# Kernel optimization log

Measured on AMD Instinct MI355X. Metric: run time of the kernel, lower is better.

Reference implementation:

```python
import jax, jax.numpy as jnp
import numpy as np

RES = 64; UP = 128; LATENT = 16; RGB_LAT = 15
XYZ_MIN = -1.0; XYZ_MAX = 1.0
STEPSIZE = 0.5; NEAR = 0.2; FAR = 6.0; BG = 1.0
VOXEL = (XYZ_MAX - XYZ_MIN) / RES
ALPHA_INIT = 1e-4
ACT_SHIFT = float(np.log(1.0 / (1.0 - ALPHA_INIT) - 1.0))
N_SAMPLES = int(np.linalg.norm(np.array([2 * RES + 1] * 3)) / STEPSIZE) + 1
BN_SCALE = (1.0 + 1e-5) ** -0.5  # eval-mode BatchNorm with running_mean=0, running_var=1
EPS = 1e-12
FREQS = [float(2.0 ** i) for i in range(6)]

def _sobel_kernel():
    hd = np.array([-1., -2., 0., 2., 1.]); h = np.array([1., 4., 6., 4., 1.])
    kx = np.einsum('i,j,k->ijk', hd, h, h)
    ky = np.einsum('i,j,k->ijk', h, hd, h)
    kz = np.einsum('i,j,k->ijk', h, h, hd)
    K = np.stack([kx, ky, kz])[:, None]
    return jnp.asarray(K / np.abs(K).max(), dtype=jnp.float32)

SOBEL_K = _sobel_kernel()

def _normalize(x, axis=-1):
    return x / jnp.maximum(jnp.linalg.norm(x, axis=axis, keepdims=True), EPS)

def _conv1x1(x, w, b):
    return jnp.einsum('oc,cdhw->odhw', w, x) + b[:, None, None, None]

def _bn(x, g, b):
    return x * (BN_SCALE * g)[:, None, None, None] + b[:, None, None, None]

def _prelu(x, a):
    return jnp.where(x >= 0, x, a[:, None, None, None] * x)

def _grid_reg(grid, c1_w, c1_b, bn1_g, bn1_b, pr1_a, c2_w, c2_b, bn2_g, bn2_b, pr2_a, c3_w, c3_b):
    x1 = _prelu(_bn(_conv1x1(grid, c1_w, c1_b), bn1_g, bn1_b), pr1_a)
    x2 = _prelu(_bn(_conv1x1(jnp.concatenate([x1, grid], 0), c2_w, c2_b), bn2_g, bn2_b), pr2_a)
    x3 = _conv1x1(jnp.concatenate([x1, x2, grid], 0), c3_w, c3_b)  # [(1+15)*8, R, R, R]
    # PixelShuffle3d(scale=2): [16*8,R,R,R] -> [16,2R,2R,2R]
    up = x3.reshape(LATENT, 2, 2, 2, RES, RES, RES).transpose(0, 4, 1, 5, 2, 6, 3).reshape(LATENT, UP, UP, UP)
    sob = jax.lax.conv_general_dilated(up[:1][None], SOBEL_K, (1, 1, 1), [(2, 2)] * 3,
                                       dimension_numbers=('NCDHW', 'OIDHW', 'NCDHW'))[0]
    normals = -_normalize(sob, axis=0)
    return up.transpose(1, 2, 3, 0), normals.transpose(1, 2, 3, 0)  # [UP,UP,UP,16], [UP,UP,UP,3]

def _trilinear(feat, p):
    # feat: [UP,UP,UP,C] indexed as world (x,y,z); p: [...,3] world coords. align_corners=True.
    u = jnp.clip((p - XYZ_MIN) / (XYZ_MAX - XYZ_MIN) * (UP - 1), 0.0, UP - 1.0)
    i0 = jnp.clip(jnp.floor(u).astype(jnp.int32), 0, UP - 2)
    f = u - i0.astype(u.dtype)
    ix, iy, iz = i0[..., 0], i0[..., 1], i0[..., 2]
    fx, fy, fz = f[..., 0:1], f[..., 1:2], f[..., 2:3]
    def g(dx, dy, dz):
        return feat[ix + dx, iy + dy, iz + dz]
    c00 = g(0, 0, 0) * (1 - fz) + g(0, 0, 1) * fz
    c01 = g(0, 1, 0) * (1 - fz) + g(0, 1, 1) * fz
    c10 = g(1, 0, 0) * (1 - fz) + g(1, 0, 1) * fz
    c11 = g(1, 1, 0) * (1 - fz) + g(1, 1, 1) * fz
    c0 = c00 * (1 - fy) + c01 * fy
    c1 = c10 * (1 - fy) + c11 * fy
    return c0 * (1 - fx) + c1 * fx

def _sample_ray(rays_o, rays_d):
    vec = jnp.where(rays_d == 0, 1e-6, rays_d)
    rate_a = (XYZ_MAX - rays_o) / vec
    rate_b = (XYZ_MIN - rays_o) / vec
    t_min = jnp.clip(jnp.minimum(rate_a, rate_b).max(-1), NEAR, FAR)
    t_max = jnp.clip(jnp.maximum(rate_a, rate_b).min(-1), NEAR, FAR)
    mask_ray = t_max <= t_min
    rng = jnp.arange(N_SAMPLES, dtype=rays_o.dtype)  # eval mode: no jitter
    step = STEPSIZE * VOXEL * rng
    interpx = t_min[:, None] + step[None] / jnp.linalg.norm(rays_d, axis=-1, keepdims=True)
    pts = rays_o[:, None, :] + rays_d[:, None, :] * interpx[..., None]
    outbox = mask_ray[:, None] | ((pts < XYZ_MIN) | (pts > XYZ_MAX)).any(-1)
    return pts, outbox

def _forward(rays_o, rays_d, viewdirs, grid, c1_w, c1_b, bn1_g, bn1_b, pr1_a, c2_w, c2_b, bn2_g, bn2_b, pr2_a, c3_w, c3_b, mlp_w0, mlp_b0, mlp_w1, mlp_b1, mlp_w2, mlp_b2, mlp_w3, mlp_b3):
    feat_grid, normals_grid = _grid_reg(grid, c1_w, c1_b, bn1_g, bn1_b, pr1_a, c2_w, c2_b, bn2_g, bn2_b, pr2_a, c3_w, c3_b)
    pts, outbox = _sample_ray(rays_o, rays_d)
    inside = ~outbox
    N, S = pts.shape[:2]
    pf = pts.reshape(-1, 3)

    def alpha_fn(p):
        d = _trilinear(feat_grid, p)[..., 0]
        return 1.0 - jnp.exp(-jax.nn.softplus(d + ACT_SHIFT) * STEPSIZE)

    alpha_flat, vjp_fn = jax.vjp(alpha_fn, pf)
    grads = vjp_fn(jnp.ones_like(alpha_flat))[0]  # d alpha / d point (analytic normals)
    nd = -_normalize(grads).reshape(N, S, 3)
    nd = jnp.where(inside[..., None], nd, 0.0)
    alpha = jnp.where(inside, alpha_flat.reshape(N, S), 0.0)

    feat = _trilinear(feat_grid, pf)
    rgb_latent = feat[:, 1:].reshape(N, S, RGB_LAT)

    ns = -_normalize(_trilinear(normals_grid, pf)).reshape(N, S, 3)  # sobel normals
    ns = jnp.where(inside[..., None], ns, 0.0)

    v = jnp.broadcast_to(viewdirs[:, None, :], nd.shape)
    dot = jnp.sum(-v * nd, -1, keepdims=True)
    refdirs = 2.0 * dot * nd + v
    emb = jnp.concatenate([refdirs] + [f(refdirs * fr) for fr in FREQS for f in (jnp.sin, jnp.cos)], -1)
    hfeat = jnp.concatenate([rgb_latent, emb], -1)  # [N,S,54]
    h = jax.nn.relu(hfeat @ mlp_w0 + mlp_b0)
    h = jax.nn.relu(h @ mlp_w1 + mlp_b1)
    h = jax.nn.relu(h @ mlp_w2 + mlp_b2)
    rgb = jax.nn.sigmoid(h @ mlp_w3 + mlp_b3)
    rgb = jnp.where(inside[..., None], rgb, 0.0)

    t = jnp.cumprod(jnp.clip(1.0 - alpha, 1e-10, None), -1)
    alphainv = jnp.concatenate([jnp.ones_like(t[..., :1]), t], -1)
    weights = alpha * alphainv[..., :-1]
    rgb_m = (weights[..., None] * rgb).sum(-2) + alphainv[..., -1:] * BG
    depth = jnp.linalg.norm(rays_o[:, None, :] - pts, axis=-1)
    depth_m = (weights * depth).sum(-1) + alphainv[..., -1] * FAR
    disp = 1.0 / depth_m
    acc = weights.sum(-1)
    nm = (weights[..., None] * nd).sum(-2)
    sm = (weights[..., None] * ns).sum(-2)
    return jnp.concatenate([rgb_m, depth_m[..., None], disp[..., None], acc[..., None], nm, sm], -1)  # [N,12]

def setup_inputs() -> dict:
    key = jax.random.key(0)
    ks = jax.random.split(key, 16)
    N = 1024
    cam = jnp.array([0.0, 0.0, -2.5], dtype=jnp.float32)
    rays_o = cam + 0.05 * jax.random.normal(ks[0], (N, 3), dtype=jnp.float32)
    tgt = jax.random.uniform(ks[1], (N, 3), minval=-0.5, maxval=0.5, dtype=jnp.float32)
    d = tgt - rays_o
    viewdirs = d / jnp.linalg.norm(d, axis=-1, keepdims=True)
    def w(k, shape, s=0.1):
        return s * jax.random.normal(k, shape, dtype=jnp.float32)
    return dict(
        rays_o=rays_o, rays_d=d, viewdirs=viewdirs,
        grid=w(ks[2], (16, 64, 64, 64)),
        c1_w=w(ks[3], (64, 16)), c1_b=w(ks[4], (64,), 0.01),
        bn1_g=jnp.ones(64, jnp.float32), bn1_b=jnp.zeros(64, jnp.float32), pr1_a=0.25 * jnp.ones(64, jnp.float32),
        c2_w=w(ks[5], (64, 80)), c2_b=w(ks[6], (64,), 0.01),
        bn2_g=jnp.ones(64, jnp.float32), bn2_b=jnp.zeros(64, jnp.float32), pr2_a=0.25 * jnp.ones(64, jnp.float32),
        c3_w=w(ks[7], (128, 144)), c3_b=w(ks[8], (128,), 0.01),
        mlp_w0=w(ks[9], (54, 64)), mlp_b0=jnp.zeros(64, jnp.float32),
        mlp_w1=w(ks[10], (64, 64)), mlp_b1=jnp.zeros(64, jnp.float32),
        mlp_w2=w(ks[11], (64, 64)), mlp_b2=jnp.zeros(64, jnp.float32),
        mlp_w3=w(ks[12], (64, 3)), mlp_b3=jnp.zeros(3, jnp.float32))

def reference(rays_o, rays_d, viewdirs, grid, c1_w, c1_b, bn1_g, bn1_b, pr1_a, c2_w, c2_b, bn2_g, bn2_b, pr2_a, c3_w, c3_b, mlp_w0, mlp_b0, mlp_w1, mlp_b1, mlp_w2, mlp_b2, mlp_w3, mlp_b3):
    return _forward(rays_o, rays_d, viewdirs, grid, c1_w, c1_b, bn1_g, bn1_b, pr1_a, c2_w, c2_b, bn2_g, bn2_b, pr2_a, c3_w, c3_b, mlp_w0, mlp_b0, mlp_w1, mlp_b1, mlp_w2, mlp_b2, mlp_w3, mlp_b3)
```

## Files before the change

kernel.cpp:

```cpp
#include <hip/hip_runtime.h>
#include <math.h>

#define S_SAMPLES 447
#define ACT_SHIFT -9.210240366971207f
#define BN_SCALE_C 0.9999950000374997f
#define STEP_VOX 0.015625f

__device__ __forceinline__ unsigned f2bf_u(float f) {
    unsigned u = __float_as_uint(f);
    return (u + 0x7fffu + ((u >> 16) & 1u)) >> 16;
}
__device__ __forceinline__ float bf2f(unsigned short u) {
    return __uint_as_float(((unsigned)u) << 16);
}
__device__ __forceinline__ float bf_lo(unsigned u) { return __uint_as_float(u << 16); }
__device__ __forceinline__ float bf_hi(unsigned u) { return __uint_as_float(u & 0xffff0000u); }

typedef __attribute__((ext_vector_type(8))) short bf16x8;
typedef __attribute__((ext_vector_type(4))) float f32x4;

__global__ __launch_bounds__(256) void prep_kernel(
    const float* __restrict__ w1, const float* __restrict__ w2,
    const float* __restrict__ w3, const float* __restrict__ b3,
    const float* __restrict__ mw0, const float* __restrict__ mw1,
    const float* __restrict__ mw2,
    unsigned short* __restrict__ w1b, unsigned short* __restrict__ w2b,
    unsigned short* __restrict__ w3b, float* __restrict__ b3p,
    unsigned short* __restrict__ m0t, unsigned short* __restrict__ m1t,
    unsigned short* __restrict__ m2t)
{
    const int gid = blockIdx.x * 256 + threadIdx.x;
    const int gs = gridDim.x * 256;
    for (int idx = gid; idx < 2048; idx += gs) {
        const int o = idx >> 5, k = idx & 31;
        w1b[idx] = (k < 16) ? (unsigned short)f2bf_u(w1[o * 16 + k]) : 0;
    }
    for (int idx = gid; idx < 6144; idx += gs) {
        const int o = idx / 96, k = idx % 96;
        w2b[idx] = (k < 80) ? (unsigned short)f2bf_u(w2[o * 80 + k]) : 0;
    }
    for (int idx = gid; idx < 20480; idx += gs) {
        const int n = idx / 160, k = idx % 160;
        const int s = n >> 4, l = n & 15;
        const int o = l * 8 + s;
        float val = 0.f;
        if (k < 64)       val = w3[o * 144 + k];
        else if (k < 80)  val = w3[o * 144 + 128 + (k - 64)];
        else if (k >= 96) val = w3[o * 144 + 64 + (k - 96)];
        w3b[idx] = (unsigned short)f2bf_u(val);
    }
    for (int idx = gid; idx < 128; idx += gs) {
        const int o = idx;
        b3p[(o & 7) * 16 + (o >> 3)] = b3[o];
    }
    for (int idx = gid; idx < 4096; idx += gs) {
        const int o = idx >> 6, k = idx & 63;
        m0t[o * 64 + k] = (k < 54) ? (unsigned short)f2bf_u(mw0[k * 64 + o]) : 0;
    }
    for (int idx = gid; idx < 4096; idx += gs) {
        const int o = idx >> 6, k = idx & 63;
        m1t[o * 64 + k] = (unsigned short)f2bf_u(mw1[k * 64 + o]);
    }
    for (int idx = gid; idx < 4096; idx += gs) {
        const int o = idx >> 6, k = idx & 63;
        m2t[o * 64 + k] = (unsigned short)f2bf_u(mw2[k * 64 + o]);
    }
}

__global__ __launch_bounds__(64) void conv_fused_kernel(
    const float* __restrict__ grid,
    const unsigned short* __restrict__ w1b, const float* __restrict__ b1,
    const float* __restrict__ g1, const float* __restrict__ bb1, const float* __restrict__ a1,
    const unsigned short* __restrict__ w2b, const float* __restrict__ b2,
    const float* __restrict__ g2, const float* __restrict__ bb2, const float* __restrict__ a2,
    const unsigned short* __restrict__ w3b, const float* __restrict__ b3p,
    unsigned short* __restrict__ featb, float* __restrict__ dens)
{
    __shared__ __align__(16) unsigned short AT[32 * 168];
    __shared__ float densT[32 * 8];
    unsigned short* Ct = AT;
    const int t = threadIdx.x;
    const int v0 = blockIdx.x * 32;

    for (int idx = t; idx < 256; idx += 64) {
        const int v = idx >> 3, c = idx & 7;
        *(unsigned*)(AT + v * 168 + 80 + c * 2) = 0;
    }
#pragma unroll
    for (int i = 0; i < 8; ++i) {
        const int c = 2 * i + (t >> 5);
        const float gv = grid[(size_t)c * 262144 + v0 + (t & 31)];
        AT[(t & 31) * 168 + 64 + c] = (unsigned short)f2bf_u(gv);
    }
    __syncthreads();

    const int quad = t >> 4, l16 = t & 15;

    {
        f32x4 acc[2][4];
        float gs[4], bb[4], al[4];
#pragma unroll
        for (int nt = 0; nt < 4; ++nt) {
            const int ch = 16 * nt + l16;
            const float bch = b1[ch];
            gs[nt] = BN_SCALE_C * g1[ch]; bb[nt] = bb1[ch]; al[nt] = a1[ch];
#pragma unroll
            for (int mt = 0; mt < 2; ++mt) {
                acc[mt][nt][0] = bch; acc[mt][nt][1] = bch;
                acc[mt][nt][2] = bch; acc[mt][nt][3] = bch;
            }
        }
        const int k0 = 8 * quad;
        bf16x8 a[2], b[4];
#pragma unroll
        for (int mt = 0; mt < 2; ++mt)
            a[mt] = __builtin_bit_cast(bf16x8, *(const uint4*)(AT + (16 * mt + l16) * 168 + 64 + k0));
#pragma unroll
        for (int nt = 0; nt < 4; ++nt)
            b[nt] = __builtin_bit_cast(bf16x8, *(const uint4*)(w1b + (16 * nt + l16) * 32 + k0));
#pragma unroll
        for (int mt = 0; mt < 2; ++mt)
#pragma unroll
            for (int nt = 0; nt < 4; ++nt)
                acc[mt][nt] = __builtin_amdgcn_mfma_f32_16x16x32_bf16(a[mt], b[nt], acc[mt][nt], 0, 0, 0);
        __syncthreads();
#pragma unroll
        for (int mt = 0; mt < 2; ++mt)
#pragma unroll
            for (int nt = 0; nt < 4; ++nt)
#pragma unroll
                for (int reg = 0; reg < 4; ++reg) {
                    float x = acc[mt][nt][reg] * gs[nt] + bb[nt];
                    x = (x >= 0.f) ? x : al[nt] * x;
                    AT[(16 * mt + 4 * quad + reg) * 168 + 16 * nt + l16] = (unsigned short)f2bf_u(x);
                }
    }
    __syncthreads();

    {
        f32x4 acc[2][4];
        float gs[4], bb[4], al[4];
#pragma unroll
        for (int nt = 0; nt < 4; ++nt) {
            const int ch = 16 * nt + l16;
            const float bch = b2[ch];
            gs[nt] = BN_SCALE_C * g2[ch]; bb[nt] = bb2[ch]; al[nt] = a2[ch];
#pragma unroll
            for (int mt = 0; mt < 2; ++mt) {
                acc[mt][nt][0] = bch; acc[mt][nt][1] = bch;
                acc[mt][nt][2] = bch; acc[mt][nt][3] = bch;
            }
        }
#pragma unroll
        for (int kq = 0; kq < 3; ++kq) {
            const int k0 = 32 * kq + 8 * quad;
            bf16x8 a[2], b[4];
#pragma unroll
            for (int mt = 0; mt < 2; ++mt)
                a[mt] = __builtin_bit_cast(bf16x8, *(const uint4*)(AT + (16 * mt + l16) * 168 + k0));
#pragma unroll
            for (int nt = 0; nt < 4; ++nt)
                b[nt] = __builtin_bit_cast(bf16x8, *(const uint4*)(w2b + (16 * nt + l16) * 96 + k0));
#pragma unroll
            for (int mt = 0; mt < 2; ++mt)
#pragma unroll
                for (int nt = 0; nt < 4; ++nt)
                    acc[mt][nt] = __builtin_amdgcn_mfma_f32_16x16x32_bf16(a[mt], b[nt], acc[mt][nt], 0, 0, 0);
        }
        __syncthreads();
#pragma unroll
        for (int mt = 0; mt < 2; ++mt)
#pragma unroll
            for (int nt = 0; nt < 4; ++nt)
#pragma unroll
                for (int reg = 0; reg < 4; ++reg) {
                    float x = acc[mt][nt][reg] * gs[nt] + bb[nt];
                    x = (x >= 0.f) ? x : al[nt] * x;
                    AT[(16 * mt + 4 * quad + reg) * 168 + 96 + 16 * nt + l16] = (unsigned short)f2bf_u(x);
                }
    }
    __syncthreads();

    {
        f32x4 acc[2][8];
#pragma unroll
        for (int nt = 0; nt < 8; ++nt) {
            const float bv = b3p[16 * nt + l16];
#pragma unroll
            for (int mt = 0; mt < 2; ++mt) {
                acc[mt][nt][0] = bv; acc[mt][nt][1] = bv;
                acc[mt][nt][2] = bv; acc[mt][nt][3] = bv;
            }
        }
#pragma unroll
        for (int kq = 0; kq < 5; ++kq) {
            const int k0 = 32 * kq + 8 * quad;
            bf16x8 a[2], b[8];
#pragma unroll
            for (int mt = 0; mt < 2; ++mt)
                a[mt] = __builtin_bit_cast(bf16x8, *(const uint4*)(AT + (16 * mt + l16) * 168 + k0));
#pragma unroll
            for (int nt = 0; nt < 8; ++nt)
                b[nt] = __builtin_bit_cast(bf16x8, *(const uint4*)(w3b + (size_t)(16 * nt + l16) * 160 + k0));
#pragma unroll
            for (int mt = 0; mt < 2; ++mt)
#pragma unroll
                for (int nt = 0; nt < 8; ++nt)
                    acc[mt][nt] = __builtin_amdgcn_mfma_f32_16x16x32_bf16(a[mt], b[nt], acc[mt][nt], 0, 0, 0);
        }

        __syncthreads();

        if (l16 == 0) {
#pragma unroll
            for (int mt = 0; mt < 2; ++mt)
#pragma unroll
                for (int nt = 0; nt < 8; ++nt)
#pragma unroll
                    for (int reg = 0; reg < 4; ++reg)
                        densT[(16 * mt + 4 * quad + reg) * 8 + nt] = acc[mt][nt][reg];
        }
#pragma unroll
        for (int mt = 0; mt < 2; ++mt)
#pragma unroll
            for (int nt = 0; nt < 8; ++nt)
#pragma unroll
                for (int reg = 0; reg < 4; ++reg)
                    Ct[(16 * mt + 4 * quad + reg) * 136 + 16 * nt + l16] =
                        (unsigned short)f2bf_u(acc[mt][nt][reg]);
    }
    __syncthreads();

    const int v = t >> 1, half = t & 1;
    const int vg = v0 + v;
    const int Z = vg & 63, Y = (vg >> 6) & 63, X = vg >> 12;
#pragma unroll
    for (int si = 0; si < 4; ++si) {
        const int s = 4 * half + si;
        const int d2 = (s >> 2) & 1, h2 = (s >> 1) & 1, w2i = s & 1;
        const int ubase = ((2 * X + d2) * 128 + (2 * Y + h2)) * 128 + (2 * Z + w2i);
        const uint4 q0 = *(const uint4*)(Ct + v * 136 + 16 * s);
        const uint4 q1 = *(const uint4*)(Ct + v * 136 + 16 * s + 8);
        *(uint4*)(featb + (size_t)ubase * 16)     = q0;
        *(uint4*)(featb + (size_t)ubase * 16 + 8) = q1;
        dens[ubase] = densT[v * 8 + s];
    }
}

__global__ __launch_bounds__(256) void sobelZ_kernel(const float* __restrict__ dens,
                                                     float2* __restrict__ zbuf)
{
    const int v = blockIdx.x * 256 + threadIdx.x;
    const int z = v & 127;
    float d[5];
#pragma unroll
    for (int k = 0; k < 5; ++k) {
        const int zz = z + k - 2;
        d[k] = (zz >= 0 && zz < 128) ? dens[v + (k - 2)] : 0.f;
    }
    const float az = d[0] + 4.f * d[1] + 6.f * d[2] + 4.f * d[3] + d[4];
    const float bz = -d[0] - 2.f * d[1] + 2.f * d[3] + d[4];
    zbuf[v] = make_float2(az, bz);
}

__global__ __launch_bounds__(256) void sobelY_kernel(const float2* __restrict__ zbuf,
                                                     float4* __restrict__ cbuf)
{
    const int v = blockIdx.x * 256 + threadIdx.x;
    const int y = (v >> 7) & 127;
    float2 e[5];
#pragma unroll
    for (int j = 0; j < 5; ++j) {
        const int yy = y + j - 2;
        e[j] = (yy >= 0 && yy < 128) ? zbuf[v + (j - 2) * 128] : make_float2(0.f, 0.f);
    }
    const float c1 = e[0].x + 4.f * e[1].x + 6.f * e[2].x + 4.f * e[3].x + e[4].x;
    const float c2 = -e[0].x - 2.f * e[1].x + 2.f * e[3].x + e[4].x;
    const float c3 = e[0].y + 4.f * e[1].y + 6.f * e[2].y + 4.f * e[3].y + e[4].y;
    cbuf[v] = make_float4(c1, c2, c3, 0.f);
}

__global__ __launch_bounds__(256) void sobelX_kernel(const float4* __restrict__ cbuf,
                                                     float* __restrict__ normals)
{
    const int v = blockIdx.x * 256 + threadIdx.x;
    const int x = v >> 14;
    float4 q[5];
#pragma unroll
    for (int i = 0; i < 5; ++i) {
        const int xx = x + i - 2;
        q[i] = (xx >= 0 && xx < 128) ? cbuf[v + (i - 2) * 16384]
                                     : make_float4(0.f, 0.f, 0.f, 0.f);
    }
    float sx = -q[0].x - 2.f * q[1].x + 2.f * q[3].x + q[4].x;
    float sy = q[0].y + 4.f * q[1].y + 6.f * q[2].y + 4.f * q[3].y + q[4].y;
    float sz = q[0].z + 4.f * q[1].z + 6.f * q[2].z + 4.f * q[3].z + q[4].z;
    sx *= (1.f / 72.f); sy *= (1.f / 72.f); sz *= (1.f / 72.f);
    const float n = sqrtf(sx * sx + sy * sy + sz * sz);
    const float inv = 1.f / fmaxf(n, 1e-12f);
    normals[v * 3 + 0] = -sx * inv;
    normals[v * 3 + 1] = -sy * inv;
    normals[v * 3 + 2] = -sz * inv;
}

__device__ __forceinline__ void mfma_layer(unsigned short* A,
                                           const unsigned short* __restrict__ Wg,
                                           const float* __restrict__ bias,
                                           const int lane)
{
    const int quad = lane >> 4, l16 = lane & 15;
    f32x4 acc[4][4];
#pragma unroll
    for (int nt = 0; nt < 4; ++nt) {
        const float bv = bias[16 * nt + l16];
#pragma unroll
        for (int mt = 0; mt < 4; ++mt) {
            acc[mt][nt][0] = bv; acc[mt][nt][1] = bv;
            acc[mt][nt][2] = bv; acc[mt][nt][3] = bv;
        }
    }
    bf16x8 a[2][4], b[2][4];
#pragma unroll
    for (int kq = 0; kq < 2; ++kq) {
        const int k0 = 32 * kq + 8 * quad;
#pragma unroll
        for (int mt = 0; mt < 4; ++mt)
            a[kq][mt] = __builtin_bit_cast(bf16x8, *(const uint4*)(A + (16 * mt + l16) * 72 + k0));
#pragma unroll
        for (int nt = 0; nt < 4; ++nt)
            b[kq][nt] = __builtin_bit_cast(bf16x8, *(const uint4*)(Wg + (16 * nt + l16) * 64 + k0));
    }
#pragma unroll
    for (int kq = 0; kq < 2; ++kq)
#pragma unroll
        for (int mt = 0; mt < 4; ++mt)
#pragma unroll
            for (int nt = 0; nt < 4; ++nt)
                acc[mt][nt] = __builtin_amdgcn_mfma_f32_16x16x32_bf16(a[kq][mt], b[kq][nt], acc[mt][nt], 0, 0, 0);
    __syncthreads();
#pragma unroll
    for (int mt = 0; mt < 4; ++mt)
#pragma unroll
        for (int nt = 0; nt < 4; ++nt)
#pragma unroll
            for (int reg = 0; reg < 4; ++reg) {
                const float v = fmaxf(acc[mt][nt][reg], 0.f);
                A[(16 * mt + 4 * quad + reg) * 72 + 16 * nt + l16] =
                    (unsigned short)f2bf_u(v);
            }
    __syncthreads();
}

__global__ __launch_bounds__(64) void sample_kernel(
    const float* __restrict__ ro, const float* __restrict__ rd, const float* __restrict__ vd,
    const unsigned short* __restrict__ featb, const float* __restrict__ dens,
    const float* __restrict__ normals,
    const unsigned short* __restrict__ m0t, const float* __restrict__ mb0,
    const unsigned short* __restrict__ m1t, const float* __restrict__ mb1,
    const unsigned short* __restrict__ m2t, const float* __restrict__ mb2,
    const float* __restrict__ mw3, const float* __restrict__ mb3,
    float* __restrict__ sbuf, const int total)
{
    __shared__ __align__(16) unsigned short act[64 * 72];

    const int t = threadIdx.x;
    const int s = blockIdx.x * 64 + t;
    const bool live = (s < total);
    bool actv = false;
    float alpha = 0.f, ndx = 0.f, ndy = 0.f, ndz = 0.f;
    float nsx = 0.f, nsy = 0.f, nsz = 0.f, depth = 0.f;
    float hf[64];
#pragma unroll
    for (int q = 0; q < 64; ++q) hf[q] = 0.f;

    if (live) {
        const int r = s / S_SAMPLES;
        const int j = s - r * S_SAMPLES;

        const float ox = ro[r * 3 + 0], oy = ro[r * 3 + 1], oz = ro[r * 3 + 2];
        const float dx = rd[r * 3 + 0], dy = rd[r * 3 + 1], dz = rd[r * 3 + 2];
        const float vx = vd[r * 3 + 0], vy = vd[r * 3 + 1], vz = vd[r * 3 + 2];

        const float vecx = (dx == 0.f) ? 1e-6f : dx;
        const float vecy = (dy == 0.f) ? 1e-6f : dy;
        const float vecz = (dz == 0.f) ? 1e-6f : dz;
        const float rax = (1.f - ox) / vecx, rbx = (-1.f - ox) / vecx;
        const float ray2 = (1.f - oy) / vecy, rby = (-1.f - oy) / vecy;
        const float raz = (1.f - oz) / vecz, rbz = (-1.f - oz) / vecz;
        float tmin = fmaxf(fmaxf(fminf(rax, rbx), fminf(ray2, rby)), fminf(raz, rbz));
        float tmax = fminf(fminf(fmaxf(rax, rbx), fmaxf(ray2, rby)), fmaxf(raz, rbz));
        tmin = fminf(fmaxf(tmin, 0.2f), 6.0f);
        tmax = fminf(fmaxf(tmax, 0.2f), 6.0f);
        const bool mask_ray = (tmax <= tmin);

        const float ndr = sqrtf(dx * dx + dy * dy + dz * dz);
        const float interpx = tmin + (STEP_VOX * (float)j) / ndr;
        const float px = ox + dx * interpx;
        const float py = oy + dy * interpx;
        const float pz = oz + dz * interpx;
        const bool outbox = mask_ray || (px < -1.f) || (px > 1.f) || (py < -1.f) ||
                            (py > 1.f) || (pz < -1.f) || (pz > 1.f);
        actv = !outbox;
        if (actv) {
            const float ux = fminf(fmaxf((px + 1.f) * 63.5f, 0.f), 127.f);
            const float uy = fminf(fmaxf((py + 1.f) * 63.5f, 0.f), 127.f);
            const float uz = fminf(fmaxf((pz + 1.f) * 63.5f, 0.f), 127.f);
            const int ix = min(max((int)floorf(ux), 0), 126);
            const int iy = min(max((int)floorf(uy), 0), 126);
            const int iz = min(max((int)floorf(uz), 0), 126);
            const float fx = ux - (float)ix, fy = uy - (float)iy, fz = uz - (float)iz;

            float lat[15];
#pragma unroll
            for (int q = 0; q < 15; ++q) lat[q] = 0.f;
            float na0 = 0.f, na1 = 0.f, na2 = 0.f;
            float c0v[8];
#pragma unroll
            for (int cn = 0; cn < 8; ++cn) {
                const int adx = cn >> 2, ady = (cn >> 1) & 1, adz = cn & 1;
                const int vox = ((ix + adx) * 128 + (iy + ady)) * 128 + (iz + adz);
                const float w = (adx ? fx : 1.f - fx) * (ady ? fy : 1.f - fy) * (adz ? fz : 1.f - fz);
                c0v[cn] = dens[vox];
                const uint4* cp = (const uint4*)(featb + (size_t)vox * 16);
                const uint4 q0 = cp[0], q1 = cp[1];
                lat[0]  = fmaf(w, bf_hi(q0.x), lat[0]);
                lat[1]  = fmaf(w, bf_lo(q0.y), lat[1]);
                lat[2]  = fmaf(w, bf_hi(q0.y), lat[2]);
                lat[3]  = fmaf(w, bf_lo(q0.z), lat[3]);
                lat[4]  = fmaf(w, bf_hi(q0.z), lat[4]);
                lat[5]  = fmaf(w, bf_lo(q0.w), lat[5]);
                lat[6]  = fmaf(w, bf_hi(q0.w), lat[6]);
                lat[7]  = fmaf(w, bf_lo(q1.x), lat[7]);
                lat[8]  = fmaf(w, bf_hi(q1.x), lat[8]);
                lat[9]  = fmaf(w, bf_lo(q1.y), lat[9]);
                lat[10] = fmaf(w, bf_hi(q1.y), lat[10]);
                lat[11] = fmaf(w, bf_lo(q1.z), lat[11]);
                lat[12] = fmaf(w, bf_hi(q1.z), lat[12]);
                lat[13] = fmaf(w, bf_lo(q1.w), lat[13]);
                lat[14] = fmaf(w, bf_hi(q1.w), lat[14]);
                const float* np_ = normals + (size_t)vox * 3;
                na0 = fmaf(w, np_[0], na0);
                na1 = fmaf(w, np_[1], na1);
                na2 = fmaf(w, np_[2], na2);
            }

            const float c00 = c0v[0] * (1.f - fz) + c0v[1] * fz;
            const float c01 = c0v[2] * (1.f - fz) + c0v[3] * fz;
            const float c10 = c0v[4] * (1.f - fz) + c0v[5] * fz;
            const float c11 = c0v[6] * (1.f - fz) + c0v[7] * fz;
            const float e0 = c00 * (1.f - fy) + c01 * fy;
            const float e1 = c10 * (1.f - fy) + c11 * fy;
            const float d0 = e0 * (1.f - fx) + e1 * fx;
            const float dfx = e1 - e0;
            const float dfy = (c01 - c00) * (1.f - fx) + (c11 - c10) * fx;
            const float dfz = ((c0v[1] - c0v[0]) * (1.f - fy) + (c0v[3] - c0v[2]) * fy) * (1.f - fx)
                            + ((c0v[5] - c0v[4]) * (1.f - fy) + (c0v[7] - c0v[6]) * fy) * fx;

            const float zin = d0 + ACT_SHIFT;
            const float splus = fmaxf(zin, 0.f) + log1pf(__expf(-fabsf(zin)));
            const float e = __expf(-splus * 0.5f);
            alpha = 1.f - e;
            const float sig = 1.f / (1.f + __expf(-zin));
            const float dad = e * 0.5f * sig;
            const float gx = dad * dfx * 63.5f;
            const float gy = dad * dfy * 63.5f;
            const float gz = dad * dfz * 63.5f;
            const float gn = sqrtf(gx * gx + gy * gy + gz * gz);
            const float gi = 1.f / fmaxf(gn, 1e-12f);
            ndx = -gx * gi; ndy = -gy * gi; ndz = -gz * gi;

            const float nn = sqrtf(na0 * na0 + na1 * na1 + na2 * na2);
            const float ni = 1.f / fmaxf(nn, 1e-12f);
            nsx = -na0 * ni; nsy = -na1 * ni; nsz = -na2 * ni;

            const float dotv = -(vx * ndx + vy * ndy + vz * ndz);
            const float rx = 2.f * dotv * ndx + vx;
            const float ry = 2.f * dotv * ndy + vy;
            const float rz = 2.f * dotv * ndz + vz;

#pragma unroll
            for (int q = 0; q < 15; ++q) hf[q] = lat[q];
            hf[15] = rx; hf[16] = ry; hf[17] = rz;
#pragma unroll
            for (int fi = 0; fi < 6; ++fi) {
                const float fr = (float)(1 << fi);
                hf[18 + fi * 6 + 0] = __sinf(rx * fr);
                hf[18 + fi * 6 + 1] = __sinf(ry * fr);
                hf[18 + fi * 6 + 2] = __sinf(rz * fr);
                hf[18 + fi * 6 + 3] = __cosf(rx * fr);
                hf[18 + fi * 6 + 4] = __cosf(ry * fr);
                hf[18 + fi * 6 + 5] = __cosf(rz * fr);
            }
            depth = interpx * ndr;
        }
    }

#pragma unroll
    for (int q = 0; q < 8; ++q) {
        uint4 st;
        st.x = f2bf_u(hf[8 * q + 0]) | (f2bf_u(hf[8 * q + 1]) << 16);
        st.y = f2bf_u(hf[8 * q + 2]) | (f2bf_u(hf[8 * q + 3]) << 16);
        st.z = f2bf_u(hf[8 * q + 4]) | (f2bf_u(hf[8 * q + 5]) << 16);
        st.w = f2bf_u(hf[8 * q + 6]) | (f2bf_u(hf[8 * q + 7]) << 16);
        *(uint4*)(act + t * 72 + 8 * q) = st;
    }
    __syncthreads();

    mfma_layer(act, m0t, mb0, t);
    mfma_layer(act, m1t, mb1, t);
    mfma_layer(act, m2t, mb2, t);

    if (live) {
        float* so = sbuf + (size_t)s * 12;
        if (actv) {
            float r0 = mb3[0], r1 = mb3[1], r2 = mb3[2];
            const unsigned short* hr = act + t * 72;
#pragma unroll
            for (int c8 = 0; c8 < 8; ++c8) {
                const uint4 hu = *(const uint4*)(hr + 8 * c8);
                const float h[8] = {bf_lo(hu.x), bf_hi(hu.x), bf_lo(hu.y), bf_hi(hu.y),
                                    bf_lo(hu.z), bf_hi(hu.z), bf_lo(hu.w), bf_hi(hu.w)};
#pragma unroll
                for (int u = 0; u < 8; ++u) {
                    const int c = 8 * c8 + u;
                    r0 = fmaf(h[u], mw3[c * 3 + 0], r0);
                    r1 = fmaf(h[u], mw3[c * 3 + 1], r1);
                    r2 = fmaf(h[u], mw3[c * 3 + 2], r2);
                }
            }
            so[0] = alpha;
            so[1] = 1.f / (1.f + __expf(-r0));
            so[2] = 1.f / (1.f + __expf(-r1));
            so[3] = 1.f / (1.f + __expf(-r2));
            so[4] = ndx; so[5] = ndy; so[6] = ndz;
            so[7] = nsx; so[8] = nsy; so[9] = nsz;
            so[10] = depth;
            so[11] = 0.f;
        } else {
#pragma unroll
            for (int q = 0; q < 12; ++q) so[q] = 0.f;
        }
    }
}

__global__ __launch_bounds__(64) void reduce_kernel(const float* __restrict__ sbuf,
                                                    float* __restrict__ out)
{
    const int r = blockIdx.x;
    const int lane = threadIdx.x;
    const int per = (S_SAMPLES + 63) / 64;
    const int j0 = lane * per;
    const int j1 = min(S_SAMPLES, j0 + per);

    float p = 1.f;
    for (int j = j0; j < j1; ++j) {
        const float a = sbuf[((size_t)r * S_SAMPLES + j) * 12];
        p *= fmaxf(1.f - a, 1e-10f);
    }
    float scan = p;
#pragma unroll
    for (int off = 1; off < 64; off <<= 1) {
        const float nv = __shfl_up(scan, (unsigned)off, 64);
        if (lane >= off) scan *= nv;
    }
    const float total = __shfl(scan, 63, 64);
    float pref = __shfl_up(scan, 1u, 64);
    if (lane == 0) pref = 1.f;

    float s0 = 0, s1 = 0, s2 = 0, s3 = 0, s4 = 0, s5 = 0, s6 = 0, s7 = 0, s8 = 0, s9 = 0, s10 = 0;
    for (int j = j0; j < j1; ++j) {
        const float* sp_ = sbuf + ((size_t)r * S_SAMPLES + j) * 12;
        const float a = sp_[0];
        const float w = a * pref;
        pref *= fmaxf(1.f - a, 1e-10f);
        s0 = fmaf(w, sp_[1], s0);
        s1 = fmaf(w, sp_[2], s1);
        s2 = fmaf(w, sp_[3], s2);
        s3 = fmaf(w, sp_[10], s3);
        s4 += w;
        s5 = fmaf(w, sp_[4], s5);
        s6 = fmaf(w, sp_[5], s6);
        s7 = fmaf(w, sp_[6], s7);
        s8 = fmaf(w, sp_[7], s8);
        s9 = fmaf(w, sp_[8], s9);
        s10 = fmaf(w, sp_[9], s10);
    }
#pragma unroll
    for (int m = 32; m >= 1; m >>= 1) {
        s0 += __shfl_xor(s0, m, 64);
        s1 += __shfl_xor(s1, m, 64);
        s2 += __shfl_xor(s2, m, 64);
        s3 += __shfl_xor(s3, m, 64);
        s4 += __shfl_xor(s4, m, 64);
        s5 += __shfl_xor(s5, m, 64);
        s6 += __shfl_xor(s6, m, 64);
        s7 += __shfl_xor(s7, m, 64);
        s8 += __shfl_xor(s8, m, 64);
        s9 += __shfl_xor(s9, m, 64);
        s10 += __shfl_xor(s10, m, 64);
    }
    if (lane == 0) {
        const float dm = s3 + total * 6.0f;
        out[r * 12 + 0] = s0 + total;
        out[r * 12 + 1] = s1 + total;
        out[r * 12 + 2] = s2 + total;
        out[r * 12 + 3] = dm;
        out[r * 12 + 4] = 1.f / dm;
        out[r * 12 + 5] = s4;
        out[r * 12 + 6] = s5; out[r * 12 + 7] = s6; out[r * 12 + 8] = s7;
        out[r * 12 + 9] = s8; out[r * 12 + 10] = s9; out[r * 12 + 11] = s10;
    }
}

extern "C" void kernel_launch(void* const* d_in, const int* in_sizes, int n_in,
                              void* d_out, int out_size, void* d_ws, size_t ws_size,
                              hipStream_t stream)
{
    (void)n_in; (void)out_size; (void)ws_size;
    const float* rays_o   = (const float*)d_in[0];
    const float* rays_d   = (const float*)d_in[1];
    const float* viewdirs = (const float*)d_in[2];
    const float* grid     = (const float*)d_in[3];
    const float* c1_w  = (const float*)d_in[4];
    const float* c1_b  = (const float*)d_in[5];
    const float* bn1_g = (const float*)d_in[6];
    const float* bn1_b = (const float*)d_in[7];
    const float* pr1_a = (const float*)d_in[8];
    const float* c2_w  = (const float*)d_in[9];
    const float* c2_b  = (const float*)d_in[10];
    const float* bn2_g = (const float*)d_in[11];
    const float* bn2_b = (const float*)d_in[12];
    const float* pr2_a = (const float*)d_in[13];
    const float* c3_w  = (const float*)d_in[14];
    const float* c3_b  = (const float*)d_in[15];
    const float* mw0 = (const float*)d_in[16];
    const float* mb0 = (const float*)d_in[17];
    const float* mw1 = (const float*)d_in[18];
    const float* mb1 = (const float*)d_in[19];
    const float* mw2 = (const float*)d_in[20];
    const float* mb2 = (const float*)d_in[21];
    const float* mw3 = (const float*)d_in[22];
    const float* mb3 = (const float*)d_in[23];

    const int N = in_sizes[0] / 3;
    const int total = N * S_SAMPLES;

    float* wsf = (float*)d_ws;
    unsigned short* featb = (unsigned short*)wsf;
    float* dens    = wsf + (size_t)16777216;
    float* normals = wsf + (size_t)18874368;
    float2* zbuf   = (float2*)(wsf + (size_t)25165824);
    float4* cbuf   = (float4*)(wsf + (size_t)29360128);
    float* sbuf    = wsf + (size_t)39845888;
    float* b3p = wsf + (size_t)45337600;
    unsigned short* w1b = (unsigned short*)(wsf + (size_t)45337728);
    unsigned short* w2b = (unsigned short*)(wsf + (size_t)45338752);
    unsigned short* w3b = (unsigned short*)(wsf + (size_t)45341824);
    unsigned short* m0t = (unsigned short*)(wsf + (size_t)45352064);
    unsigned short* m1t = (unsigned short*)(wsf + (size_t)45354112);
    unsigned short* m2t = (unsigned short*)(wsf + (size_t)45356160);

    prep_kernel<<<64, 256, 0, stream>>>(c1_w, c2_w, c3_w, c3_b, mw0, mw1, mw2,
                                        w1b, w2b, w3b, b3p, m0t, m1t, m2t);
    conv_fused_kernel<<<8192, 64, 0, stream>>>(grid, w1b, c1_b, bn1_g, bn1_b, pr1_a,
                                               w2b, c2_b, bn2_g, bn2_b, pr2_a,
                                               w3b, b3p, featb, dens);
    sobelZ_kernel<<<8192, 256, 0, stream>>>(dens, zbuf);
    sobelY_kernel<<<8192, 256, 0, stream>>>(zbuf, cbuf);
    sobelX_kernel<<<8192, 256, 0, stream>>>(cbuf, normals);
    const int sblocks = (total + 63) / 64;
    sample_kernel<<<sblocks, 64, 0, stream>>>(rays_o, rays_d, viewdirs, featb, dens, normals,
                                              m0t, mb0, m1t, mb1, m2t, mb2, mw3, mb3,
                                              sbuf, total);
    reduce_kernel<<<N, 64, 0, stream>>>(sbuf, (float*)d_out);
}
```

Measured before the change: 242.9 us.

## Process four voxel tiles per conv block with register-prefetched grid loads

The fused conv kernel now loops over four 32-voxel tiles per block, launching a quarter as many blocks. Per-channel BN/PReLU/bias parameters are loaded once per block, and the next tile's grid values are prefetched into registers while the current tile computes. This amortizes parameter loads and hides global-load latency, at the cost of fewer blocks (2048 single-wave blocks) and more register pressure, which may reduce latency hiding through occupancy.

```diff
diff --git a/kernel.cpp b/kernel.cpp
--- a/kernel.cpp
+++ b/kernel.cpp
@@ -5,6 +5,7 @@
 #define ACT_SHIFT -9.210240366971207f
 #define BN_SCALE_C 0.9999950000374997f
 #define STEP_VOX 0.015625f
+#define CTILES 4
 
 __device__ __forceinline__ unsigned f2bf_u(float f) {
     unsigned u = __float_as_uint(f);
@@ -80,171 +81,189 @@
     __shared__ float densT[32 * 8];
     unsigned short* Ct = AT;
     const int t = threadIdx.x;
-    const int v0 = blockIdx.x * 32;
-
-    for (int idx = t; idx < 256; idx += 64) {
-        const int v = idx >> 3, c = idx & 7;
-        *(unsigned*)(AT + v * 168 + 80 + c * 2) = 0;
-    }
-#pragma unroll
-    for (int i = 0; i < 8; ++i) {
-        const int c = 2 * i + (t >> 5);
-        const float gv = grid[(size_t)c * 262144 + v0 + (t & 31)];
-        AT[(t & 31) * 168 + 64 + c] = (unsigned short)f2bf_u(gv);
-    }
-    __syncthreads();
-
     const int quad = t >> 4, l16 = t & 15;
-
-    {
-        f32x4 acc[2][4];
-        float gs[4], bb[4], al[4];
-#pragma unroll
-        for (int nt = 0; nt < 4; ++nt) {
-            const int ch = 16 * nt + l16;
-            const float bch = b1[ch];
-            gs[nt] = BN_SCALE_C * g1[ch]; bb[nt] = bb1[ch]; al[nt] = a1[ch];
-#pragma unroll
-            for (int mt = 0; mt < 2; ++mt) {
-                acc[mt][nt][0] = bch; acc[mt][nt][1] = bch;
-                acc[mt][nt][2] = bch; acc[mt][nt][3] = bch;
-            }
-        }
-        const int k0 = 8 * quad;
-        bf16x8 a[2], b[4];
-#pragma unroll
-        for (int mt = 0; mt < 2; ++mt)
-            a[mt] = __builtin_bit_cast(bf16x8, *(const uint4*)(AT + (16 * mt + l16) * 168 + 64 + k0));
-#pragma unroll
-        for (int nt = 0; nt < 4; ++nt)
-            b[nt] = __builtin_bit_cast(bf16x8, *(const uint4*)(w1b + (16 * nt + l16) * 32 + k0));
-#pragma unroll
-        for (int mt = 0; mt < 2; ++mt)
+    const int gc = 2 * 0 + (t >> 5);
+    const int gv = t & 31;
+
+    float gs1[4], bb1v[4], al1[4], bch1[4];
+    float gs2[4], bb2v[4], al2[4], bch2[4];
+    float b3v[8];
+#pragma unroll
+    for (int nt = 0; nt < 4; ++nt) {
+        const int ch = 16 * nt + l16;
+        bch1[nt] = b1[ch]; gs1[nt] = BN_SCALE_C * g1[ch]; bb1v[nt] = bb1[ch]; al1[nt] = a1[ch];
+        bch2[nt] = b2[ch]; gs2[nt] = BN_SCALE_C * g2[ch]; bb2v[nt] = bb2[ch]; al2[nt] = a2[ch];
+    }
+#pragma unroll
+    for (int nt = 0; nt < 8; ++nt) b3v[nt] = b3p[16 * nt + l16];
+
+    const int vblock = blockIdx.x * (32 * CTILES);
+
+    float gpre[8];
+#pragma unroll
+    for (int i = 0; i < 8; ++i)
+        gpre[i] = grid[(size_t)(2 * i + (t >> 5)) * 262144 + vblock + gv];
+
+#pragma unroll 1
+    for (int tile = 0; tile < CTILES; ++tile) {
+        const int v0 = vblock + 32 * tile;
+        __syncthreads();
+
+        for (int idx = t; idx < 256; idx += 64) {
+            const int v = idx >> 3, c = idx & 7;
+            *(unsigned*)(AT + v * 168 + 80 + c * 2) = 0;
+        }
+#pragma unroll
+        for (int i = 0; i < 8; ++i) {
+            const int c = 2 * i + (t >> 5);
+            AT[gv * 168 + 64 + c] = (unsigned short)f2bf_u(gpre[i]);
+        }
+        if (tile + 1 < CTILES) {
+#pragma unroll
+            for (int i = 0; i < 8; ++i)
+                gpre[i] = grid[(size_t)(2 * i + (t >> 5)) * 262144 + v0 + 32 + gv];
+        }
+        __syncthreads();
+
+        {
+            f32x4 acc[2][4];
 #pragma unroll
             for (int nt = 0; nt < 4; ++nt)
-                acc[mt][nt] = __builtin_amdgcn_mfma_f32_16x16x32_bf16(a[mt], b[nt], acc[mt][nt], 0, 0, 0);
-        __syncthreads();
-#pragma unroll
-        for (int mt = 0; mt < 2; ++mt)
+#pragma unroll
+                for (int mt = 0; mt < 2; ++mt) {
+                    acc[mt][nt][0] = bch1[nt]; acc[mt][nt][1] = bch1[nt];
+                    acc[mt][nt][2] = bch1[nt]; acc[mt][nt][3] = bch1[nt];
+                }
+            const int k0 = 8 * quad;
+            bf16x8 a[2], b[4];
+#pragma unroll
+            for (int mt = 0; mt < 2; ++mt)
+                a[mt] = __builtin_bit_cast(bf16x8, *(const uint4*)(AT + (16 * mt + l16) * 168 + 64 + k0));
 #pragma unroll
             for (int nt = 0; nt < 4; ++nt)
-#pragma unroll
-                for (int reg = 0; reg < 4; ++reg) {
-                    float x = acc[mt][nt][reg] * gs[nt] + bb[nt];
-                    x = (x >= 0.f) ? x : al[nt] * x;
-                    AT[(16 * mt + 4 * quad + reg) * 168 + 16 * nt + l16] = (unsigned short)f2bf_u(x);
-                }
-    }
-    __syncthreads();
-
-    {
-        f32x4 acc[2][4];
-        float gs[4], bb[4], al[4];
-#pragma unroll
-        for (int nt = 0; nt < 4; ++nt) {
-            const int ch = 16 * nt + l16;
-            const float bch = b2[ch];
-            gs[nt] = BN_SCALE_C * g2[ch]; bb[nt] = bb2[ch]; al[nt] = a2[ch];
-#pragma unroll
-            for (int mt = 0; mt < 2; ++mt) {
-                acc[mt][nt][0] = bch; acc[mt][nt][1] = bch;
-                acc[mt][nt][2] = bch; acc[mt][nt][3] = bch;
-            }
-        }
-#pragma unroll
-        for (int kq = 0; kq < 3; ++kq) {
-            const int k0 = 32 * kq + 8 * quad;
-            bf16x8 a[2], b[4];
-#pragma unroll
-            for (int mt = 0; mt < 2; ++mt)
-                a[mt] = __builtin_bit_cast(bf16x8, *(const uint4*)(AT + (16 * mt + l16) * 168 + k0));
-#pragma unroll
-            for (int nt = 0; nt < 4; ++nt)
-                b[nt] = __builtin_bit_cast(bf16x8, *(const uint4*)(w2b + (16 * nt + l16) * 96 + k0));
+                b[nt] = __builtin_bit_cast(bf16x8, *(const uint4*)(w1b + (16 * nt + l16) * 32 + k0));
 #pragma unroll
             for (int mt = 0; mt < 2; ++mt)
 #pragma unroll
                 for (int nt = 0; nt < 4; ++nt)
                     acc[mt][nt] = __builtin_amdgcn_mfma_f32_16x16x32_bf16(a[mt], b[nt], acc[mt][nt], 0, 0, 0);
+            __syncthreads();
+#pragma unroll
+            for (int mt = 0; mt < 2; ++mt)
+#pragma unroll
+                for (int nt = 0; nt < 4; ++nt)
+#pragma unroll
+                    for (int reg = 0; reg < 4; ++reg) {
+                        float x = acc[mt][nt][reg] * gs1[nt] + bb1v[nt];
+                        x = (x >= 0.f) ? x : al1[nt] * x;
+                        AT[(16 * mt + 4 * quad + reg) * 168 + 16 * nt + l16] = (unsigned short)f2bf_u(x);
+                    }
         }
         __syncthreads();
-#pragma unroll
-        for (int mt = 0; mt < 2; ++mt)
+
+        {
+            f32x4 acc[2][4];
 #pragma unroll
             for (int nt = 0; nt < 4; ++nt)
 #pragma unroll
-                for (int reg = 0; reg < 4; ++reg) {
-                    float x = acc[mt][nt][reg] * gs[nt] + bb[nt];
-                    x = (x >= 0.f) ? x : al[nt] * x;
-                    AT[(16 * mt + 4 * quad + reg) * 168 + 96 + 16 * nt + l16] = (unsigned short)f2bf_u(x);
+                for (int mt = 0; mt < 2; ++mt) {
+                    acc[mt][nt][0] = bch2[nt]; acc[mt][nt][1] = bch2[nt];
+                    acc[mt][nt][2] = bch2[nt]; acc[mt][nt][3] = bch2[nt];
                 }
-    }
-    __syncthreads();
-
-    {
-        f32x4 acc[2][8];
-#pragma unroll
-        for (int nt = 0; nt < 8; ++nt) {
-            const float bv = b3p[16 * nt + l16];
-#pragma unroll
-            for (int mt = 0; mt < 2; ++mt) {
-                acc[mt][nt][0] = bv; acc[mt][nt][1] = bv;
-                acc[mt][nt][2] = bv; acc[mt][nt][3] = bv;
+#pragma unroll
+            for (int kq = 0; kq < 3; ++kq) {
+                const int k0 = 32 * kq + 8 * quad;
+                bf16x8 a[2], b[4];
+#pragma unroll
+                for (int mt = 0; mt < 2; ++mt)
+                    a[mt] = __builtin_bit_cast(bf16x8, *(const uint4*)(AT + (16 * mt + l16) * 168 + k0));
+#pragma unroll
+                for (int nt = 0; nt < 4; ++nt)
+                    b[nt] = __builtin_bit_cast(bf16x8, *(const uint4*)(w2b + (16 * nt + l16) * 96 + k0));
+#pragma unroll
+                for (int mt = 0; mt < 2; ++mt)
+#pragma unroll
+                    for (int nt = 0; nt < 4; ++nt)
+                        acc[mt][nt] = __builtin_amdgcn_mfma_f32_16x16x32_bf16(a[mt], b[nt], acc[mt][nt], 0, 0, 0);
             }
-        }
-#pragma unroll
-        for (int kq = 0; kq < 5; ++kq) {
-            const int k0 = 32 * kq + 8 * quad;
-            bf16x8 a[2], b[8];
+            __syncthreads();
 #pragma unroll
             for (int mt = 0; mt < 2; ++mt)
-                a[mt] = __builtin_bit_cast(bf16x8, *(const uint4*)(AT + (16 * mt + l16) * 168 + k0));
+#pragma unroll
+                for (int nt = 0; nt < 4; ++nt)
+#pragma unroll
+                    for (int reg = 0; reg < 4; ++reg) {
+                        float x = acc[mt][nt][reg] * gs2[nt] + bb2v[nt];
+                        x = (x >= 0.f) ? x : al2[nt] * x;
+                        AT[(16 * mt + 4 * quad + reg) * 168 + 96 + 16 * nt + l16] = (unsigned short)f2bf_u(x);
+                    }
+        }
+        __syncthreads();
+
+        {
+            f32x4 acc[2][8];
 #pragma unroll
             for (int nt = 0; nt < 8; ++nt)
-                b[nt] = __builtin_bit_cast(bf16x8, *(const uint4*)(w3b + (size_t)(16 * nt + l16) * 160 + k0));
+#pragma unroll
+                for (int mt = 0; mt < 2; ++mt) {
+                    acc[mt][nt][0] = b3v[nt]; acc[mt][nt][1] = b3v[nt];
+                    acc[mt][nt][2] = b3v[nt]; acc[mt][nt][3] = b3v[nt];
+                }
+#pragma unroll
+            for (int kq = 0; kq < 5; ++kq) {
+                const int k0 = 32 * kq + 8 * quad;
+                bf16x8 a[2], b[8];
+#pragma unroll
+                for (int mt = 0; mt < 2; ++mt)
+                    a[mt] = __builtin_bit_cast(bf16x8, *(const uint4*)(AT + (16 * mt + l16) * 168 + k0));
+#pragma unroll
+                for (int nt = 0; nt < 8; ++nt)
+                    b[nt] = __builtin_bit_cast(bf16x8, *(const uint4*)(w3b + (size_t)(16 * nt + l16) * 160 + k0));
+#pragma unroll
+                for (int mt = 0; mt < 2; ++mt)
+#pragma unroll
+                    for (int nt = 0; nt < 8; ++nt)
+                        acc[mt][nt] = __builtin_amdgcn_mfma_f32_16x16x32_bf16(a[mt], b[nt], acc[mt][nt], 0, 0, 0);
+            }
+
+            __syncthreads();
+
+            if (l16 == 0) {
+#pragma unroll
+                for (int mt = 0; mt < 2; ++mt)
+#pragma unroll
+                    for (int nt = 0; nt < 8; ++nt)
+#pragma unroll
+                        for (int reg = 0; reg < 4; ++reg)
+                            densT[(16 * mt + 4 * quad + reg) * 8 + nt] = acc[mt][nt][reg];
+            }
 #pragma unroll
             for (int mt = 0; mt < 2; ++mt)
 #pragma unroll
                 for (int nt = 0; nt < 8; ++nt)
-                    acc[mt][nt] = __builtin_amdgcn_mfma_f32_16x16x32_bf16(a[mt], b[nt], acc[mt][nt], 0, 0, 0);
-        }
-
+#pragma unroll
+                    for (int reg = 0; reg < 4; ++reg)
+                        Ct[(16 * mt + 4 * quad + reg) * 136 + 16 * nt + l16] =
+                            (unsigned short)f2bf_u(acc[mt][nt][reg]);
+        }
         __syncthreads();
 
-        if (l16 == 0) {
-#pragma unroll
-            for (int mt = 0; mt < 2; ++mt)
-#pragma unroll
-                for (int nt = 0; nt < 8; ++nt)
-#pragma unroll
-                    for (int reg = 0; reg < 4; ++reg)
-                        densT[(16 * mt + 4 * quad + reg) * 8 + nt] = acc[mt][nt][reg];
-        }
-#pragma unroll
-        for (int mt = 0; mt < 2; ++mt)
-#pragma unroll
-            for (int nt = 0; nt < 8; ++nt)
-#pragma unroll
-                for (int reg = 0; reg < 4; ++reg)
-                    Ct[(16 * mt + 4 * quad + reg) * 136 + 16 * nt + l16] =
-                        (unsigned short)f2bf_u(acc[mt][nt][reg]);
-    }
-    __syncthreads();
-
-    const int v = t >> 1, half = t & 1;
-    const int vg = v0 + v;
-    const int Z = vg & 63, Y = (vg >> 6) & 63, X = vg >> 12;
-#pragma unroll
-    for (int si = 0; si < 4; ++si) {
-        const int s = 4 * half + si;
-        const int d2 = (s >> 2) & 1, h2 = (s >> 1) & 1, w2i = s & 1;
-        const int ubase = ((2 * X + d2) * 128 + (2 * Y + h2)) * 128 + (2 * Z + w2i);
-        const uint4 q0 = *(const uint4*)(Ct + v * 136 + 16 * s);
-        const uint4 q1 = *(const uint4*)(Ct + v * 136 + 16 * s + 8);
-        *(uint4*)(featb + (size_t)ubase * 16)     = q0;
-        *(uint4*)(featb + (size_t)ubase * 16 + 8) = q1;
-        dens[ubase] = densT[v * 8 + s];
-    }
+        const int v = t >> 1, half = t & 1;
+        const int vg = v0 + v;
+        const int Z = vg & 63, Y = (vg >> 6) & 63, X = vg >> 12;
+#pragma unroll
+        for (int si = 0; si < 4; ++si) {
+            const int s = 4 * half + si;
+            const int d2 = (s >> 2) & 1, h2 = (s >> 1) & 1, w2i = s & 1;
+            const int ubase = ((2 * X + d2) * 128 + (2 * Y + h2)) * 128 + (2 * Z + w2i);
+            const uint4 q0 = *(const uint4*)(Ct + v * 136 + 16 * s);
+            const uint4 q1 = *(const uint4*)(Ct + v * 136 + 16 * s + 8);
+            *(uint4*)(featb + (size_t)ubase * 16)     = q0;
+            *(uint4*)(featb + (size_t)ubase * 16 + 8) = q1;
+            dens[ubase] = densT[v * 8 + s];
+        }
+    }
+    (void)gc;
 }
 
 __global__ __launch_bounds__(256) void sobelZ_kernel(const float* __restrict__ dens,
@@ -662,9 +681,9 @@
 
     prep_kernel<<<64, 256, 0, stream>>>(c1_w, c2_w, c3_w, c3_b, mw0, mw1, mw2,
                                         w1b, w2b, w3b, b3p, m0t, m1t, m2t);
-    conv_fused_kernel<<<8192, 64, 0, stream>>>(grid, w1b, c1_b, bn1_g, bn1_b, pr1_a,
-                                               w2b, c2_b, bn2_g, bn2_b, pr2_a,
-                                               w3b, b3p, featb, dens);
+    conv_fused_kernel<<<8192 / CTILES, 64, 0, stream>>>(grid, w1b, c1_b, bn1_g, bn1_b, pr1_a,
+                                                        w2b, c2_b, bn2_g, bn2_b, pr2_a,
+                                                        w3b, b3p, featb, dens);
     sobelZ_kernel<<<8192, 256, 0, stream>>>(dens, zbuf);
     sobelY_kernel<<<8192, 256, 0, stream>>>(zbuf, cbuf);
     sobelX_kernel<<<8192, 256, 0, stream>>>(cbuf, normals);
```

Result: no change. 243.1 us (+0.1%).
